# Optimization experiments

Hardware: AMD Instinct MI355X
Metric: run time of the kernel (lower is better)

## Reference

```python
import jax, jax.numpy as jnp
import numpy as np

B, L, D, H, N = 8, 2048, 128, 4, 2
DK = D // H          # 32
DFF = 2 * D          # 256 (dff = d * 2 in source)


def _init_proj(key, shape):
    # matches torch init: uniform in [-s, s], s = sqrt(6/(fan_in+fan_out)) of last two dims
    s = np.sqrt(6.0 / (shape[-1] + shape[-2]))
    return jax.random.uniform(key, shape, jnp.float32, -s, s)


def setup_inputs() -> dict:
    key = jax.random.key(0)
    ks = jax.random.split(key, 8)
    x = jax.random.normal(ks[0], (B, L, D), jnp.float32)
    mask = jnp.ones((B, L), jnp.float32)
    Wq = _init_proj(ks[1], (N, H, D, DK))
    Wk = _init_proj(ks[2], (N, H, D, DK))
    Wv = _init_proj(ks[3], (N, H, D, DK))
    Wo = _init_proj(ks[4], (N, H * DK, D))
    W1 = _init_proj(ks[5], (N, D, DFF))
    b1 = jnp.zeros((N, 1, 1, DFF), jnp.float32)
    W2 = _init_proj(ks[6], (N, DFF, D))
    b2 = jnp.zeros((N, 1, 1, D), jnp.float32)
    return {"x": x, "mask": mask, "Wq": Wq, "Wk": Wk, "Wv": Wv,
            "Wo": Wo, "W1": W1, "b1": b1, "W2": W2, "b2": b2}


def reference(x, mask, Wq, Wk, Wv, Wo, W1, b1, W2, b2):
    # Eval-mode forward (no attention dropout-mask trick, no FFN dropout).
    neg = jnp.finfo(x.dtype).min
    m2 = mask[:, :, None] * mask[:, None, :]              # [B, L, L]
    add_mask = (1.0 - m2)[:, None, :, :] * neg            # [B, 1, L, L]
    bsz, max_len, _ = x.shape
    for i in range(N):  # small fixed layer loop
        q = jnp.einsum('bld,hde->bhle', x, Wq[i])         # [B,H,L,DK]
        k = jnp.einsum('bld,hde->bhle', x, Wk[i])
        v = jnp.einsum('bld,hde->bhle', x, Wv[i])
        A = jnp.einsum('bhqe,bhke->bhqk', q, k) + add_mask  # note: no 1/sqrt(dk), as in source
        A = jax.nn.softmax(A, axis=-1)                    # [B,H,L,L]
        o = jnp.einsum('bhqk,bhke->bqhe', A, v)           # [B,L,H,DK]
        o = o.reshape(bsz, max_len, H * DK) @ Wo[i]       # [B,L,D]
        x = (o + x) / 2
        f = jax.nn.gelu(x @ W1[i] + b1[i], approximate=False)  # torch F.gelu is exact erf
        f = f @ W2[i] + b2[i]
        x = (f + x) / 2
    return x
```

## Files before the change

### kernel.cpp

```cpp
#include <hip/hip_runtime.h>
#include <math.h>

#define BB 8
#define LL 2048
#define DD 128
#define HH 4
#define DKK 32
#define DFFF 256

#define NEGMIN (-3.402823466e38f)
#define LOG2E 1.44269504088896f

typedef _Float16 f16;
typedef _Float16 f16x4 __attribute__((ext_vector_type(4)));
typedef _Float16 f16x8 __attribute__((ext_vector_type(8)));
typedef __fp16 h16x2 __attribute__((ext_vector_type(2)));
typedef float f32x4 __attribute__((ext_vector_type(4)));

union PKU { h16x2 h2[2]; f16x4 v; };

__global__ __launch_bounds__(256) void xcvt_kernel(const float* __restrict__ x,
                                                   f16* __restrict__ xh) {
  const int i = (blockIdx.x * 256 + threadIdx.x) * 8;
  float4 v0 = *(const float4*)(x + i);
  float4 v1 = *(const float4*)(x + i + 4);
  f16x8 h;
  h[0] = (f16)v0.x; h[1] = (f16)v0.y; h[2] = (f16)v0.z; h[3] = (f16)v0.w;
  h[4] = (f16)v1.x; h[5] = (f16)v1.y; h[6] = (f16)v1.z; h[7] = (f16)v1.w;
  *(f16x8*)(xh + i) = h;
}

__global__ __launch_bounds__(256) void maskchk_kernel(
    const float* __restrict__ mask, int* __restrict__ flags) {
  __shared__ int wok[4];
  const int b = blockIdx.x, t = threadIdx.x;
  bool ok = true;
  for (int i = t; i < LL; i += 256) ok &= (mask[b * LL + i] == 1.f);
  const bool all_ok = __all(ok);
  if ((t & 63) == 0) wok[t >> 6] = all_ok ? 1 : 0;
  __syncthreads();
  if (t == 0) flags[b] = wok[0] & wok[1] & wok[2] & wok[3];
}

__global__ __launch_bounds__(256) void wconv_kernel(
    const float* __restrict__ Wq, const float* __restrict__ Wk,
    const float* __restrict__ Wv, const float* __restrict__ Wo,
    const float* __restrict__ W1, const float* __restrict__ W2,
    f16* __restrict__ wt) {
  const int idx = blockIdx.x * 256 + threadIdx.x;
  const int i = idx >> 17;
  const int r = idx & 131071;
  float val;
  if (r < 49152) {
    const int sel = r / 16384;
    const int rr = r & 16383;
    const int n = rr >> 7, k = rr & 127;
    const float* W = (sel == 0) ? Wq : (sel == 1) ? Wk : Wv;
    val = W[((size_t)(i * 4 + (n >> 5)) * 128 + k) * 32 + (n & 31)];
  } else if (r < 65536) {
    const int r2 = r - 49152;
    const int n = r2 >> 7, k = r2 & 127;
    val = Wo[i * 16384 + k * 128 + n];
  } else if (r < 98304) {
    const int r2 = r - 65536;
    const int n = r2 >> 7, k = r2 & 127;
    val = W1[i * 32768 + k * 256 + n];
  } else {
    const int r2 = r - 98304;
    const int n = r2 >> 8, k = r2 & 255;
    val = W2[i * 32768 + k * 128 + n];
  }
  wt[idx] = (f16)val;
}

__global__ __launch_bounds__(256) void qkv_kernel(
    const f16* __restrict__ xh, const f16* __restrict__ wqkvT,
    f16* __restrict__ qh, f16* __restrict__ kh, f16* __restrict__ vth) {
  const int t = threadIdx.x;
  const int wave = t >> 6, lane = t & 63;
  const int g = lane >> 4, c = lane & 15;
  const int rgrp = wave >> 1, half = wave & 1;
  const int r0g = blockIdx.x * 32 + rgrp * 16;
  const int b4 = (r0g >> 11) * 4;
  const int l0 = r0g & 2047;

  f16x8 a[4];
#pragma unroll
  for (int kt = 0; kt < 4; ++kt)
    a[kt] = *(const f16x8*)(xh + (size_t)(r0g + c) * 128 + kt * 32 + g * 8);

  {
    const f16* wT = wqkvT + half * 16384;
    f16* out = (half == 0) ? qh : kh;
#pragma unroll
    for (int nt = 0; nt < 8; ++nt) {
      f32x4 acc = {0.f, 0.f, 0.f, 0.f};
#pragma unroll
      for (int kt = 0; kt < 4; ++kt) {
        f16x8 bfrag = *(const f16x8*)(wT + (nt * 16 + c) * 128 + kt * 32 + g * 8);
        acc = __builtin_amdgcn_mfma_f32_16x16x32_f16(a[kt], bfrag, acc, 0, 0, 0);
      }
      const int h = nt >> 1, e = (nt & 1) * 16 + c;
#pragma unroll
      for (int r = 0; r < 4; ++r)
        out[((size_t)(b4 + h) * LL + l0 + 4 * g + r) * DKK + e] = (f16)acc[r];
    }
  }
  {
    const f16* wT = wqkvT + 2 * 16384;
#pragma unroll
    for (int nt = 0; nt < 4; ++nt) {
      const int ntg = half * 4 + nt;
      f32x4 acc = {0.f, 0.f, 0.f, 0.f};
#pragma unroll
      for (int kt = 0; kt < 4; ++kt) {
        f16x8 afrag = *(const f16x8*)(wT + (ntg * 16 + c) * 128 + kt * 32 + g * 8);
        acc = __builtin_amdgcn_mfma_f32_16x16x32_f16(afrag, a[kt], acc, 0, 0, 0);
      }
#pragma unroll
      for (int r = 0; r < 4; ++r) {
        const int eg = ntg * 16 + 4 * g + r;
        vth[((size_t)(b4 + (eg >> 5)) * DKK + (eg & 31)) * LL + l0 + c] =
            (f16)acc[r];
      }
    }
  }
}

__global__ __launch_bounds__(256, 4) void attn_kernel(
    const f16* __restrict__ qh, const f16* __restrict__ kh,
    const f16* __restrict__ vth, const float* __restrict__ mask,
    const int* __restrict__ bflags, f16* __restrict__ o) {
  __shared__ f16 Vt[4][2][32][72];
  const int t = threadIdx.x;
  const int wave = t >> 6, lane = t & 63;
  const int g = lane >> 4, c = lane & 15;

  const int flat = blockIdx.x;
  const int xcd = flat & 7, slot = flat >> 3;
  const int bh = xcd * 4 + (slot >> 4);
  const int qb = slot & 15;
  const int b = bh >> 2;
  const int qw = qb * 128 + wave * 32;
  const bool nomask_b = (bflags[b] != 0);

  f16x8 qfrag[2];
  float mqv[2] = {1.f, 1.f};
#pragma unroll
  for (int qt = 0; qt < 2; ++qt)
    qfrag[qt] =
        *(const f16x8*)(qh + ((size_t)bh * LL + qw + qt * 16 + c) * DKK + g * 8);
  if (!nomask_b) {
#pragma unroll
    for (int qt = 0; qt < 2; ++qt) mqv[qt] = mask[b * LL + qw + qt * 16 + c];
  }

  f32x4 o4[2][2];
  float m[2], l[2];
#pragma unroll
  for (int qt = 0; qt < 2; ++qt) {
    m[qt] = -3.0e38f; l[qt] = 0.f;
#pragma unroll
    for (int dt = 0; dt < 2; ++dt)
#pragma unroll
      for (int r = 0; r < 4; ++r) o4[qt][dt][r] = 0.f;
  }

  const f16* kp = kh + (size_t)bh * LL * DKK + (size_t)c * DKK + g * 8;
  const int vd = lane >> 3, vseg = lane & 7;
  const f16* vp = vth + (size_t)bh * DKK * LL + (size_t)vd * LL + vseg * 8;

#define LOADK(DST, KT)                                       \
  {                                                          \
    const f16* _p = kp + (size_t)(KT) * 64 * DKK;            \
    DST[0] = *(const f16x8*)(_p);                            \
    DST[1] = *(const f16x8*)(_p + 16 * DKK);                 \
    DST[2] = *(const f16x8*)(_p + 32 * DKK);                 \
    DST[3] = *(const f16x8*)(_p + 48 * DKK);                 \
  }
#define LOADVREG(DST, KT)                                    \
  {                                                          \
    const f16* _p = vp + (KT) * 64;                          \
    DST[0] = *(const f16x8*)(_p);                            \
    DST[1] = *(const f16x8*)(_p + 8 * LL);                   \
    DST[2] = *(const f16x8*)(_p + 16 * LL);                  \
    DST[3] = *(const f16x8*)(_p + 24 * LL);                  \
  }
#define COMMITV(SRC, BUF)                                    \
  {                                                          \
    *(f16x8*)&Vt[wave][BUF][vd][vseg * 8] = SRC[0];          \
    *(f16x8*)&Vt[wave][BUF][vd + 8][vseg * 8] = SRC[1];      \
    *(f16x8*)&Vt[wave][BUF][vd + 16][vseg * 8] = SRC[2];     \
    *(f16x8*)&Vt[wave][BUF][vd + 24][vseg * 8] = SRC[3];     \
  }

  f16x8 kbA[4], kbB[4], vr[4];

  LOADVREG(vr, 0);
  LOADK(kbA, 0);
  COMMITV(vr, 0);

  for (int kt = 0; kt < 32; ++kt) {
    const int cur = kt & 1;
    if (kt < 31) {
      LOADK(kbB, kt + 1);
      LOADVREG(vr, kt + 1);
    }

    f32x4 st[2][4];
    __builtin_amdgcn_s_setprio(1);
#pragma unroll
    for (int qt = 0; qt < 2; ++qt)
#pragma unroll
      for (int nt = 0; nt < 4; ++nt) {
        f32x4 z = {0.f, 0.f, 0.f, 0.f};
        st[qt][nt] =
            __builtin_amdgcn_mfma_f32_16x16x32_f16(kbA[nt], qfrag[qt], z, 0, 0, 0);
      }
    __builtin_amdgcn_s_setprio(0);

    if (!nomask_b) {
      const int k0 = kt * 64;
#pragma unroll
      for (int qt = 0; qt < 2; ++qt) {
        const float mq = mqv[qt];
#pragma unroll
        for (int nt = 0; nt < 4; ++nt) {
          float4 mk4 = *(const float4*)(mask + b * LL + k0 + nt * 16 + 4 * g);
          st[qt][nt][0] += (1.f - mq * mk4.x) * NEGMIN;
          st[qt][nt][1] += (1.f - mq * mk4.y) * NEGMIN;
          st[qt][nt][2] += (1.f - mq * mk4.z) * NEGMIN;
          st[qt][nt][3] += (1.f - mq * mk4.w) * NEGMIN;
        }
      }
    }

    f16x4 va[2][4];
#pragma unroll
    for (int dt = 0; dt < 2; ++dt)
#pragma unroll
      for (int nt = 0; nt < 4; ++nt)
        va[dt][nt] = *(const f16x4*)&Vt[wave][cur][dt * 16 + c][nt * 16 + 4 * g];

#pragma unroll
    for (int qt = 0; qt < 2; ++qt) {
      float vmax = fmaxf(fmaxf(st[qt][0][0], st[qt][0][1]),
                         fmaxf(st[qt][0][2], st[qt][0][3]));
#pragma unroll
      for (int nt = 1; nt < 4; ++nt)
        vmax = fmaxf(vmax, fmaxf(fmaxf(st[qt][nt][0], st[qt][nt][1]),
                                 fmaxf(st[qt][nt][2], st[qt][nt][3])));
      vmax = fmaxf(vmax, __shfl_xor(vmax, 16));
      vmax = fmaxf(vmax, __shfl_xor(vmax, 32));

      if (!__all(vmax - m[qt] <= 8.f)) {
        const float mn = fmaxf(m[qt], vmax);
        const float sc = __builtin_exp2f((m[qt] - mn) * LOG2E);
        l[qt] *= sc;
#pragma unroll
        for (int dt = 0; dt < 2; ++dt)
#pragma unroll
          for (int r = 0; r < 4; ++r) o4[qt][dt][r] *= sc;
        m[qt] = mn;
      }
      const float mn2 = m[qt] * LOG2E;

      float p[4][4];
      float psum = 0.f;
#pragma unroll
      for (int nt = 0; nt < 4; ++nt) {
#pragma unroll
        for (int r = 0; r < 4; ++r) {
          p[nt][r] = __builtin_exp2f(fmaf(st[qt][nt][r], LOG2E, -mn2));
          psum += p[nt][r];
        }
      }
      l[qt] += psum;

      __builtin_amdgcn_s_setprio(1);
#pragma unroll
      for (int nt = 0; nt < 4; ++nt) {
        PKU pk;
        pk.h2[0] = __builtin_amdgcn_cvt_pkrtz(p[nt][0], p[nt][1]);
        pk.h2[1] = __builtin_amdgcn_cvt_pkrtz(p[nt][2], p[nt][3]);
        o4[qt][0] = __builtin_amdgcn_mfma_f32_16x16x16f16(va[0][nt], pk.v,
                                                          o4[qt][0], 0, 0, 0);
        o4[qt][1] = __builtin_amdgcn_mfma_f32_16x16x16f16(va[1][nt], pk.v,
                                                          o4[qt][1], 0, 0, 0);
      }
      __builtin_amdgcn_s_setprio(0);
    }

    if (kt < 31) {
      COMMITV(vr, 1 - cur);
#pragma unroll
      for (int i = 0; i < 4; ++i) kbA[i] = kbB[i];
    }
  }
#undef LOADK
#undef LOADVREG
#undef COMMITV

  const int h = bh & 3;
#pragma unroll
  for (int qt = 0; qt < 2; ++qt) {
    float lt = l[qt];
    lt += __shfl_xor(lt, 16);
    lt += __shfl_xor(lt, 32);
    const float rdiv = 1.f / lt;
    f16* orow = o + ((size_t)b * LL + qw + qt * 16 + c) * DD + h * DKK;
#pragma unroll
    for (int dt = 0; dt < 2; ++dt) {
      f16x4 res;
      res[0] = (f16)(o4[qt][dt][0] * rdiv);
      res[1] = (f16)(o4[qt][dt][1] * rdiv);
      res[2] = (f16)(o4[qt][dt][2] * rdiv);
      res[3] = (f16)(o4[qt][dt][3] * rdiv);
      *(f16x4*)(orow + dt * 16 + g * 4) = res;
    }
  }
}

__global__ __launch_bounds__(256) void mlp_kernel(
    const f16* __restrict__ o, const float* __restrict__ x,
    const f16* __restrict__ WoT, const f16* __restrict__ W1T,
    const f16* __restrict__ W2T, const float* __restrict__ b1,
    const float* __restrict__ b2, float* __restrict__ xout,
    const f16* __restrict__ wqkvT_next,
    f16* __restrict__ qh, f16* __restrict__ kh, f16* __restrict__ vth) {
  __shared__ f16 Xm[32][136];
  __shared__ f16 Fs[32][264];
  const int t = threadIdx.x;
  const int wave = t >> 6, lane = t & 63;
  const int g = lane >> 4, c = lane & 15;
  const int rgrp = wave >> 1, half = wave & 1;
  const int mrow = rgrp * 16;
  const long r0 = (long)blockIdx.x * 32;

  f16x8 a1[4];
#pragma unroll
  for (int kt = 0; kt < 4; ++kt)
    a1[kt] = *(const f16x8*)(o + (r0 + mrow + c) * 128 + kt * 32 + g * 8);

  f32x4 xmreg[4];
#pragma unroll
  for (int nt = 0; nt < 4; ++nt) {
    const int ntg = half * 4 + nt;
    f32x4 acc = {0.f, 0.f, 0.f, 0.f};
#pragma unroll
    for (int kt = 0; kt < 4; ++kt) {
      f16x8 bfrag = *(const f16x8*)(WoT + (ntg * 16 + c) * 128 + kt * 32 + g * 8);
      acc = __builtin_amdgcn_mfma_f32_16x16x32_f16(a1[kt], bfrag, acc, 0, 0, 0);
    }
#pragma unroll
    for (int r = 0; r < 4; ++r) {
      const float xv = x[(r0 + mrow + 4 * g + r) * 128 + ntg * 16 + c];
      acc[r] = (acc[r] + xv) * 0.5f;
      Xm[mrow + 4 * g + r][ntg * 16 + c] = (f16)acc[r];
    }
    xmreg[nt] = acc;
  }
  __syncthreads();

  f16x8 a2[4];
#pragma unroll
  for (int kt = 0; kt < 4; ++kt)
    a2[kt] = *(const f16x8*)&Xm[mrow + c][kt * 32 + g * 8];
#pragma unroll
  for (int nt = 0; nt < 8; ++nt) {
    const int ntg = half * 8 + nt;
    f32x4 acc = {0.f, 0.f, 0.f, 0.f};
#pragma unroll
    for (int kt = 0; kt < 4; ++kt) {
      f16x8 bfrag = *(const f16x8*)(W1T + (ntg * 16 + c) * 128 + kt * 32 + g * 8);
      acc = __builtin_amdgcn_mfma_f32_16x16x32_f16(a2[kt], bfrag, acc, 0, 0, 0);
    }
    const float bj = b1[ntg * 16 + c];
#pragma unroll
    for (int r = 0; r < 4; ++r) {
      const float val = acc[r] + bj;
      Fs[mrow + 4 * g + r][ntg * 16 + c] =
          (f16)(0.5f * val * (1.f + erff(val * 0.70710678118654752f)));
    }
  }
  __syncthreads();

  f16x8 a3[8];
#pragma unroll
  for (int kt = 0; kt < 8; ++kt)
    a3[kt] = *(const f16x8*)&Fs[mrow + c][kt * 32 + g * 8];
#pragma unroll
  for (int nt = 0; nt < 4; ++nt) {
    const int ntg = half * 4 + nt;
    f32x4 acc = {0.f, 0.f, 0.f, 0.f};
#pragma unroll
    for (int kt = 0; kt < 8; ++kt) {
      f16x8 bfrag = *(const f16x8*)(W2T + (ntg * 16 + c) * 256 + kt * 32 + g * 8);
      acc = __builtin_amdgcn_mfma_f32_16x16x32_f16(a3[kt], bfrag, acc, 0, 0, 0);
    }
    const float bj = b2[ntg * 16 + c];
#pragma unroll
    for (int r = 0; r < 4; ++r) {
      const float val = (acc[r] + bj + xmreg[nt][r]) * 0.5f;
      xout[(r0 + mrow + 4 * g + r) * 128 + ntg * 16 + c] = val;
      Xm[mrow + 4 * g + r][ntg * 16 + c] = (f16)val;
    }
  }

  if (wqkvT_next) {
    __syncthreads();
    const int r0g = (int)r0 + mrow;
    const int b4 = (r0g >> 11) * 4;
    const int l0 = r0g & 2047;
    f16x8 a[4];
#pragma unroll
    for (int kt = 0; kt < 4; ++kt)
      a[kt] = *(const f16x8*)&Xm[mrow + c][kt * 32 + g * 8];

    {
      const f16* wT = wqkvT_next + half * 16384;
      f16* out = (half == 0) ? qh : kh;
#pragma unroll
      for (int nt = 0; nt < 8; ++nt) {
        f32x4 acc = {0.f, 0.f, 0.f, 0.f};
#pragma unroll
        for (int kt = 0; kt < 4; ++kt) {
          f16x8 bfrag =
              *(const f16x8*)(wT + (nt * 16 + c) * 128 + kt * 32 + g * 8);
          acc = __builtin_amdgcn_mfma_f32_16x16x32_f16(a[kt], bfrag, acc, 0, 0, 0);
        }
        const int h = nt >> 1, e = (nt & 1) * 16 + c;
#pragma unroll
        for (int r = 0; r < 4; ++r)
          out[((size_t)(b4 + h) * LL + l0 + 4 * g + r) * DKK + e] = (f16)acc[r];
      }
    }
    {
      const f16* wT = wqkvT_next + 2 * 16384;
#pragma unroll
      for (int nt = 0; nt < 4; ++nt) {
        const int ntg = half * 4 + nt;
        f32x4 acc = {0.f, 0.f, 0.f, 0.f};
#pragma unroll
        for (int kt = 0; kt < 4; ++kt) {
          f16x8 afrag =
              *(const f16x8*)(wT + (ntg * 16 + c) * 128 + kt * 32 + g * 8);
          acc = __builtin_amdgcn_mfma_f32_16x16x32_f16(afrag, a[kt], acc, 0, 0, 0);
        }
#pragma unroll
        for (int r = 0; r < 4; ++r) {
          const int eg = ntg * 16 + 4 * g + r;
          vth[((size_t)(b4 + (eg >> 5)) * DKK + (eg & 31)) * LL + l0 + c] =
              (f16)acc[r];
        }
      }
    }
  }
}

extern "C" void kernel_launch(void* const* d_in, const int* in_sizes, int n_in,
                              void* d_out, int out_size, void* d_ws,
                              size_t ws_size, hipStream_t stream) {
  const float* x    = (const float*)d_in[0];
  const float* mask = (const float*)d_in[1];
  const float* Wq   = (const float*)d_in[2];
  const float* Wk   = (const float*)d_in[3];
  const float* Wv   = (const float*)d_in[4];
  const float* Wo   = (const float*)d_in[5];
  const float* W1   = (const float*)d_in[6];
  const float* b1   = (const float*)d_in[7];
  const float* W2   = (const float*)d_in[8];
  const float* b2   = (const float*)d_in[9];

  const size_t SZ = (size_t)BB * LL * DD;
  char* p = (char*)d_ws;
  f16* qh   = (f16*)p;  p += SZ * sizeof(f16);
  f16* kh   = (f16*)p;  p += SZ * sizeof(f16);
  f16* vth  = (f16*)p;  p += SZ * sizeof(f16);
  f16* ob   = (f16*)p;  p += SZ * sizeof(f16);
  f16* xh0  = (f16*)p;  p += SZ * sizeof(f16);
  f16* wt   = (f16*)p;  p += (size_t)262144 * sizeof(f16);
  int* bflags = (int*)p; p += 256;
  float* xA = (float*)p;

  wconv_kernel<<<1024, 256, 0, stream>>>(Wq, Wk, Wv, Wo, W1, W2, wt);
  xcvt_kernel<<<SZ / 8 / 256, 256, 0, stream>>>(x, xh0);
  maskchk_kernel<<<BB, 256, 0, stream>>>(mask, bflags);

  for (int i = 0; i < 2; ++i) {
    const float* xin = (i == 0) ? x : xA;
    float* xout = (i == 1) ? (float*)d_out : xA;
    const f16* qkvT_i = wt + (size_t)i * 131072;
    const f16* WoT_i  = wt + (size_t)i * 131072 + 49152;
    const f16* W1T_i  = wt + (size_t)i * 131072 + 65536;
    const f16* W2T_i  = wt + (size_t)i * 131072 + 98304;
    const float* b1_i = b1 + (long)i * DFFF;
    const float* b2_i = b2 + (long)i * DD;
    const f16* qkvT_next = (i == 0) ? (wt + 131072) : nullptr;

    if (i == 0)
      qkv_kernel<<<(BB * LL) / 32, 256, 0, stream>>>(xh0, qkvT_i, qh, kh, vth);
    attn_kernel<<<512, 256, 0, stream>>>(qh, kh, vth, mask, bflags, ob);
    mlp_kernel<<<(BB * LL) / 32, 256, 0, stream>>>(ob, xin, WoT_i, W1T_i, W2T_i,
                                                   b1_i, b2_i, xout,
                                                   qkvT_next, qh, kh, vth);
  }
}
```

Baseline: 208.8 us.

## Merge setup kernels, pad attention V tile, and tree-reduce softmax row sum

Folds the weight conversion, x fp16 conversion and mask check kernels into one launch, with blocks dispatched by index range, to remove two kernel launches and their gaps. It also widens the padding of the shared V tile row in attention from 72 to 76 halves to change the LDS bank mapping. It also replaces the serial accumulation of the softmax probability sum with a pairwise tree to shorten the dependency chain. The padding change raises LDS use per block and could alter occupancy or the alignment of vector LDS accesses.

```diff
diff --git a/kernel.cpp b/kernel.cpp
--- a/kernel.cpp
+++ b/kernel.cpp
@@ -19,58 +19,57 @@
 
 union PKU { h16x2 h2[2]; f16x4 v; };
 
-__global__ __launch_bounds__(256) void xcvt_kernel(const float* __restrict__ x,
-                                                   f16* __restrict__ xh) {
-  const int i = (blockIdx.x * 256 + threadIdx.x) * 8;
-  float4 v0 = *(const float4*)(x + i);
-  float4 v1 = *(const float4*)(x + i + 4);
-  f16x8 h;
-  h[0] = (f16)v0.x; h[1] = (f16)v0.y; h[2] = (f16)v0.z; h[3] = (f16)v0.w;
-  h[4] = (f16)v1.x; h[5] = (f16)v1.y; h[6] = (f16)v1.z; h[7] = (f16)v1.w;
-  *(f16x8*)(xh + i) = h;
-}
-
-__global__ __launch_bounds__(256) void maskchk_kernel(
-    const float* __restrict__ mask, int* __restrict__ flags) {
-  __shared__ int wok[4];
-  const int b = blockIdx.x, t = threadIdx.x;
-  bool ok = true;
-  for (int i = t; i < LL; i += 256) ok &= (mask[b * LL + i] == 1.f);
-  const bool all_ok = __all(ok);
-  if ((t & 63) == 0) wok[t >> 6] = all_ok ? 1 : 0;
-  __syncthreads();
-  if (t == 0) flags[b] = wok[0] & wok[1] & wok[2] & wok[3];
-}
-
-__global__ __launch_bounds__(256) void wconv_kernel(
+__global__ __launch_bounds__(256) void setup_kernel(
+    const float* __restrict__ x, const float* __restrict__ mask,
     const float* __restrict__ Wq, const float* __restrict__ Wk,
     const float* __restrict__ Wv, const float* __restrict__ Wo,
     const float* __restrict__ W1, const float* __restrict__ W2,
-    f16* __restrict__ wt) {
-  const int idx = blockIdx.x * 256 + threadIdx.x;
-  const int i = idx >> 17;
-  const int r = idx & 131071;
-  float val;
-  if (r < 49152) {
-    const int sel = r / 16384;
-    const int rr = r & 16383;
-    const int n = rr >> 7, k = rr & 127;
-    const float* W = (sel == 0) ? Wq : (sel == 1) ? Wk : Wv;
-    val = W[((size_t)(i * 4 + (n >> 5)) * 128 + k) * 32 + (n & 31)];
-  } else if (r < 65536) {
-    const int r2 = r - 49152;
-    const int n = r2 >> 7, k = r2 & 127;
-    val = Wo[i * 16384 + k * 128 + n];
-  } else if (r < 98304) {
-    const int r2 = r - 65536;
-    const int n = r2 >> 7, k = r2 & 127;
-    val = W1[i * 32768 + k * 256 + n];
+    f16* __restrict__ wt, f16* __restrict__ xh, int* __restrict__ flags) {
+  const int blk = blockIdx.x;
+  const int t = threadIdx.x;
+  if (blk < 1024) {
+    const int idx = blk * 256 + t;
+    const int i = idx >> 17;
+    const int r = idx & 131071;
+    float val;
+    if (r < 49152) {
+      const int sel = r / 16384;
+      const int rr = r & 16383;
+      const int n = rr >> 7, k = rr & 127;
+      const float* W = (sel == 0) ? Wq : (sel == 1) ? Wk : Wv;
+      val = W[((size_t)(i * 4 + (n >> 5)) * 128 + k) * 32 + (n & 31)];
+    } else if (r < 65536) {
+      const int r2 = r - 49152;
+      const int n = r2 >> 7, k = r2 & 127;
+      val = Wo[i * 16384 + k * 128 + n];
+    } else if (r < 98304) {
+      const int r2 = r - 65536;
+      const int n = r2 >> 7, k = r2 & 127;
+      val = W1[i * 32768 + k * 256 + n];
+    } else {
+      const int r2 = r - 98304;
+      const int n = r2 >> 8, k = r2 & 255;
+      val = W2[i * 32768 + k * 128 + n];
+    }
+    wt[idx] = (f16)val;
+  } else if (blk < 2048) {
+    const int i = ((blk - 1024) * 256 + t) * 8;
+    float4 v0 = *(const float4*)(x + i);
+    float4 v1 = *(const float4*)(x + i + 4);
+    f16x8 h;
+    h[0] = (f16)v0.x; h[1] = (f16)v0.y; h[2] = (f16)v0.z; h[3] = (f16)v0.w;
+    h[4] = (f16)v1.x; h[5] = (f16)v1.y; h[6] = (f16)v1.z; h[7] = (f16)v1.w;
+    *(f16x8*)(xh + i) = h;
   } else {
-    const int r2 = r - 98304;
-    const int n = r2 >> 8, k = r2 & 255;
-    val = W2[i * 32768 + k * 128 + n];
-  }
-  wt[idx] = (f16)val;
+    __shared__ int wok[4];
+    const int b = blk - 2048;
+    bool ok = true;
+    for (int i = t; i < LL; i += 256) ok &= (mask[b * LL + i] == 1.f);
+    const bool all_ok = __all(ok);
+    if ((t & 63) == 0) wok[t >> 6] = all_ok ? 1 : 0;
+    __syncthreads();
+    if (t == 0) flags[b] = wok[0] & wok[1] & wok[2] & wok[3];
+  }
 }
 
 __global__ __launch_bounds__(256) void qkv_kernel(
@@ -131,7 +130,7 @@
     const f16* __restrict__ qh, const f16* __restrict__ kh,
     const f16* __restrict__ vth, const float* __restrict__ mask,
     const int* __restrict__ bflags, f16* __restrict__ o) {
-  __shared__ f16 Vt[4][2][32][72];
+  __shared__ f16 Vt[4][2][32][76];
   const int t = threadIdx.x;
   const int wave = t >> 6, lane = t & 63;
   const int g = lane >> 4, c = lane & 15;
@@ -266,16 +265,16 @@
       const float mn2 = m[qt] * LOG2E;
 
       float p[4][4];
-      float psum = 0.f;
-#pragma unroll
-      for (int nt = 0; nt < 4; ++nt) {
-#pragma unroll
-        for (int r = 0; r < 4; ++r) {
+#pragma unroll
+      for (int nt = 0; nt < 4; ++nt)
+#pragma unroll
+        for (int r = 0; r < 4; ++r)
           p[nt][r] = __builtin_exp2f(fmaf(st[qt][nt][r], LOG2E, -mn2));
-          psum += p[nt][r];
-        }
-      }
-      l[qt] += psum;
+      const float s0 = (p[0][0] + p[0][1]) + (p[0][2] + p[0][3]);
+      const float s1 = (p[1][0] + p[1][1]) + (p[1][2] + p[1][3]);
+      const float s2 = (p[2][0] + p[2][1]) + (p[2][2] + p[2][3]);
+      const float s3 = (p[3][0] + p[3][1]) + (p[3][2] + p[3][3]);
+      l[qt] += (s0 + s1) + (s2 + s3);
 
       __builtin_amdgcn_s_setprio(1);
 #pragma unroll
@@ -483,9 +482,8 @@
   int* bflags = (int*)p; p += 256;
   float* xA = (float*)p;
 
-  wconv_kernel<<<1024, 256, 0, stream>>>(Wq, Wk, Wv, Wo, W1, W2, wt);
-  xcvt_kernel<<<SZ / 8 / 256, 256, 0, stream>>>(x, xh0);
-  maskchk_kernel<<<BB, 256, 0, stream>>>(mask, bflags);
+  setup_kernel<<<2056, 256, 0, stream>>>(x, mask, Wq, Wk, Wv, Wo, W1, W2,
+                                         wt, xh0, bflags);
 
   for (int i = 0; i < 2; ++i) {
     const float* xin = (i == 0) ? x : xA;
```

After: 217.1 us. 4.0% more time.
